# Kernel optimization log

Hardware: AMD Instinct MI355X
Metric: run time of the kernel (lower is better)

The kernel has to match this reference:

```python
import jax, jax.numpy as jnp
import numpy as np

B, S, H = 128, 1024, 256
NEG = 1e9

def setup_inputs() -> dict:
    key = jax.random.key(0)
    ks = jax.random.split(key, 11)
    sc = 0.05
    return {
        'ref': jax.random.normal(ks[0], (B, S, H), jnp.float32),
        'query': jax.random.normal(ks[1], (B, H), jnp.float32),
        'mask': jax.random.randint(ks[2], (B, S), 0, 2, jnp.int32),
        'wg': jax.random.normal(ks[3], (H, H), jnp.float32) * sc,
        'bg': jax.random.normal(ks[4], (H,), jnp.float32) * sc,
        'wqg': jax.random.normal(ks[5], (H, H), jnp.float32) * sc,
        'vg': jax.random.normal(ks[6], (H,), jnp.float32) * sc,
        'wp': jax.random.normal(ks[7], (H, H), jnp.float32) * sc,
        'bp': jax.random.normal(ks[8], (H,), jnp.float32) * sc,
        'wqp': jax.random.normal(ks[9], (H, H), jnp.float32) * sc,
        'vp': jax.random.normal(ks[10], (H,), jnp.float32) * sc,
    }

def reference(ref, query, mask, wg, bg, wqg, vg, wp, bp, wqp, vp):
    # Bahdanau additive pointer attention with glimpse, per PointerDecoder.pointer_net
    maskf = mask.astype(ref.dtype)
    # glimpse attention
    enc_g = jnp.einsum('bsd,hd->bsh', ref, wg) + bg            # conv1d kernel=1
    q_g = jnp.einsum('bd,hd->bh', query, wqg)                   # w_q_g (no bias)
    scores_g = jnp.einsum('bsh,h->bs', jnp.tanh(enc_g + q_g[:, None, :]), vg)
    att_g = jax.nn.softmax(scores_g - maskf * NEG, axis=-1)     # [B,S]
    glimpse = jnp.einsum('bs,bsd->bd', att_g, ref) + query      # [B,H]
    # pointer scores
    enc_p = jnp.einsum('bsd,hd->bsh', ref, wp) + bp
    q_p = jnp.einsum('bd,hd->bh', glimpse, wqp)
    scores_p = jnp.einsum('bsh,h->bs', jnp.tanh(enc_p + q_p[:, None, :]), vp)
    masked_scores = scores_p - maskf * NEG                      # [B,S]
    return masked_scores
```

## Files before the change

kernel.cpp:

```cpp
#include <hip/hip_runtime.h>

#define Bb 128
#define Ss 1024
#define Hh 256
#define NEGF 1e9f

typedef short bf16x8 __attribute__((ext_vector_type(8)));
typedef float f32x4 __attribute__((ext_vector_type(4)));

__device__ __forceinline__ short f2bf(float f) {
    union { float f; unsigned u; } c; c.f = f;
    return (short)((c.u + 0x8000u) >> 16);
}

__device__ __forceinline__ unsigned pack2bf(float lo, float hi) {
    union { float f; unsigned u; } a, b; a.f = lo; b.f = hi;
    unsigned al = (a.u + 0x8000u) >> 16;
    unsigned bh = (b.u + 0x8000u) & 0xFFFF0000u;
    return al | bh;
}

__device__ __forceinline__ float bfhi2f(unsigned u) {
    union { unsigned u; float f; } c; c.u = u & 0xFFFF0000u; return c.f;
}
__device__ __forceinline__ float bflo2f(unsigned u) {
    union { unsigned u; float f; } c; c.u = u << 16; return c.f;
}

__device__ __forceinline__ float fast_tanh(float x) {
    float cl = fminf(fmaxf(x, -10.f), 10.f);
    float e = __expf(2.f * cl);
    return (e - 1.f) * __builtin_amdgcn_rcpf(e + 1.f);
}

__device__ __forceinline__ void stage16(const short* g, short* l) {
    __builtin_amdgcn_global_load_lds((const __attribute__((address_space(1))) void*)g,
                                     (__attribute__((address_space(3))) void*)l, 16, 0, 0);
}

__global__ __launch_bounds__(256) void convert_ref(const float* __restrict__ ref,
                                                   uint4* __restrict__ refb) {
    size_t i = (size_t)blockIdx.x * 256 + threadIdx.x;
    const float4* p = (const float4*)ref + i * 2;
    float4 a = p[0], b = p[1];
    uint4 o;
    o.x = pack2bf(a.x, a.y);
    o.y = pack2bf(a.z, a.w);
    o.z = pack2bf(b.x, b.y);
    o.w = pack2bf(b.z, b.w);
    refb[i] = o;
}

__global__ __launch_bounds__(256) void convert_w(const float* __restrict__ wg,
                                                 const float* __restrict__ wp,
                                                 short* __restrict__ wgb,
                                                 short* __restrict__ wpb) {
    int i = blockIdx.x * 256 + threadIdx.x;
    wgb[i] = f2bf(wg[i]);
    wpb[i] = f2bf(wp[i]);
}

__global__ __launch_bounds__(256) void dot_qb(const float* __restrict__ q,
                                              const float* __restrict__ W,
                                              const float* __restrict__ bias,
                                              float* __restrict__ out) {
    int b = blockIdx.x, h = threadIdx.x;
    const float4* qr = (const float4*)(q + b * Hh);
    const float4* wr = (const float4*)(W + h * Hh);
    float acc = 0.f;
#pragma unroll 8
    for (int i = 0; i < Hh / 4; ++i) {
        float4 q4 = qr[i], w4 = wr[i];
        acc += q4.x * w4.x + q4.y * w4.y + q4.z * w4.z + q4.w * w4.w;
    }
    out[b * Hh + h] = acc + bias[h];
}

template <int MASKED>
__global__ __launch_bounds__(256) void scores_mfma(const short* __restrict__ refb,
                                                   const short* __restrict__ Wbf,
                                                   const float* __restrict__ qbias,
                                                   const float* __restrict__ vvec,
                                                   const int* __restrict__ mask,
                                                   float* __restrict__ out) {
    __shared__ short Wlds[2][8192];
    const int b = blockIdx.x;
    const int s0 = blockIdx.y * 128;
    const int t = threadIdx.x;
    const int wave = t >> 6;
    const int lane = t & 63;
    const int nl = lane & 15;
    const int quad = lane >> 4;
    const int rowbase = s0 + wave * 32;

    const int soff0 = (t & 15) * Hh + (t >> 6) * 32 + ((t >> 4) & 3) * 8;
    const int soff1 = soff0 + 128;
    const int dbase0 = wave * 512;
    const int dbase1 = 2048 + wave * 512;

    bf16x8 afrag[2][8];
#pragma unroll
    for (int rt = 0; rt < 2; ++rt) {
        const short* rp = refb + ((size_t)b * Ss + rowbase + rt * 16 + nl) * Hh;
#pragma unroll
        for (int kb = 0; kb < 8; ++kb)
            afrag[rt][kb] = *(const bf16x8*)(rp + kb * 32 + quad * 8);
    }

    stage16(Wbf + soff0, &Wlds[0][dbase0]);
    stage16(Wbf + soff1, &Wlds[0][dbase1]);
    stage16(Wbf + 16 * Hh + soff0, &Wlds[0][4096 + dbase0]);
    stage16(Wbf + 16 * Hh + soff1, &Wlds[0][4096 + dbase1]);
    __syncthreads();

    float sc[2][4] = {{0.f, 0.f, 0.f, 0.f}, {0.f, 0.f, 0.f, 0.f}};

    for (int nc2 = 0; nc2 < 8; ++nc2) {
        const int cur = nc2 & 1;
        if (nc2 < 7) {
            const short* g = Wbf + (size_t)(nc2 + 1) * 32 * Hh;
            stage16(g + soff0, &Wlds[1 - cur][dbase0]);
            stage16(g + soff1, &Wlds[1 - cur][dbase1]);
            stage16(g + 16 * Hh + soff0, &Wlds[1 - cur][4096 + dbase0]);
            stage16(g + 16 * Hh + soff1, &Wlds[1 - cur][4096 + dbase1]);
        }
#pragma unroll
        for (int h = 0; h < 2; ++h) {
            const int n = nc2 * 32 + h * 16 + nl;
            const float qb = qbias[b * Hh + n];
            const float vv = vvec[n];
            bf16x8 bfrag[8];
#pragma unroll
            for (int kb = 0; kb < 8; ++kb)
                bfrag[kb] = *(const bf16x8*)&Wlds[cur][h * 4096 + kb * 512 + lane * 8];
#pragma unroll
            for (int rt = 0; rt < 2; ++rt) {
                f32x4 c = {0.f, 0.f, 0.f, 0.f};
#pragma unroll
                for (int kb = 0; kb < 8; ++kb)
                    c = __builtin_amdgcn_mfma_f32_16x16x32_bf16(afrag[rt][kb], bfrag[kb], c, 0, 0, 0);
#pragma unroll
                for (int r = 0; r < 4; ++r)
                    sc[rt][r] += fast_tanh(c[r] + qb) * vv;
            }
        }
        __syncthreads();
    }

#pragma unroll
    for (int rt = 0; rt < 2; ++rt)
#pragma unroll
        for (int r = 0; r < 4; ++r) {
            float v = sc[rt][r];
            v += __shfl_xor(v, 1, 64);
            v += __shfl_xor(v, 2, 64);
            v += __shfl_xor(v, 4, 64);
            v += __shfl_xor(v, 8, 64);
            sc[rt][r] = v;
        }

    if (nl == 0) {
#pragma unroll
        for (int rt = 0; rt < 2; ++rt)
#pragma unroll
            for (int r = 0; r < 4; ++r) {
                int m = rowbase + rt * 16 + quad * 4 + r;
                float v = sc[rt][r];
                if (MASKED) v -= (float)mask[b * Ss + m] * NEGF;
                out[(size_t)b * Ss + m] = v;
            }
    }
}

__global__ __launch_bounds__(1024) void softmax_kernel(const float* __restrict__ scores,
                                                       const int* __restrict__ mask,
                                                       float* __restrict__ att) {
    int b = blockIdx.x, t = threadIdx.x;
    __shared__ float red[16];
    int idx = b * Ss + t;
    float x = scores[idx] - (float)mask[idx] * NEGF;

    float m = x;
#pragma unroll
    for (int o = 1; o < 64; o <<= 1) m = fmaxf(m, __shfl_xor(m, o, 64));
    if ((t & 63) == 0) red[t >> 6] = m;
    __syncthreads();
    float M = red[0];
#pragma unroll
    for (int j = 1; j < 16; ++j) M = fmaxf(M, red[j]);
    __syncthreads();

    float e = __expf(x - M);
    float s = e;
#pragma unroll
    for (int o = 1; o < 64; o <<= 1) s += __shfl_xor(s, o, 64);
    if ((t & 63) == 0) red[t >> 6] = s;
    __syncthreads();
    float S = 0.f;
#pragma unroll
    for (int j = 0; j < 16; ++j) S += red[j];

    att[idx] = e * __builtin_amdgcn_rcpf(S);
}

__global__ __launch_bounds__(256) void glimpse_part(const unsigned* __restrict__ refb,
                                                    const float* __restrict__ att,
                                                    float* __restrict__ gpart) {
    int b = blockIdx.x, q = blockIdx.y, t = threadIdx.x;
    const int c = t & 31;
    const int rg = t >> 5;
    __shared__ float part[8][Hh];
    const unsigned* base = refb + ((size_t)(b * Ss + q * 128)) * (Hh / 2);
    const float* ap = att + b * Ss + q * 128;

    float acc[8] = {0.f, 0.f, 0.f, 0.f, 0.f, 0.f, 0.f, 0.f};
#pragma unroll 4
    for (int it = 0; it < 16; ++it) {
        int row = it * 8 + rg;
        float a = ap[row];
        uint4 v = *(const uint4*)(base + (size_t)row * (Hh / 2) + c * 4);
        acc[0] += a * bflo2f(v.x); acc[1] += a * bfhi2f(v.x);
        acc[2] += a * bflo2f(v.y); acc[3] += a * bfhi2f(v.y);
        acc[4] += a * bflo2f(v.z); acc[5] += a * bfhi2f(v.z);
        acc[6] += a * bflo2f(v.w); acc[7] += a * bfhi2f(v.w);
    }
#pragma unroll
    for (int j = 0; j < 8; ++j) part[rg][c * 8 + j] = acc[j];
    __syncthreads();
    float s = 0.f;
#pragma unroll
    for (int g = 0; g < 8; ++g) s += part[g][t];
    gpart[(size_t)(b * 8 + q) * Hh + t] = s;
}

__global__ __launch_bounds__(256) void qbias_p_kernel(const float* __restrict__ gpart,
                                                      const float* __restrict__ query,
                                                      const float* __restrict__ wqp,
                                                      const float* __restrict__ bp,
                                                      float* __restrict__ out) {
    int b = blockIdx.x, t = threadIdx.x;
    __shared__ __align__(16) float gl[Hh];
    float g = query[b * Hh + t];
#pragma unroll
    for (int q = 0; q < 8; ++q) g += gpart[(b * 8 + q) * Hh + t];
    gl[t] = g;
    __syncthreads();
    const float4* wr = (const float4*)(wqp + t * Hh);
    const float4* gp = (const float4*)gl;
    float acc = 0.f;
#pragma unroll 8
    for (int i = 0; i < Hh / 4; ++i) {
        float4 w4 = wr[i];
        float4 g4 = gp[i];
        acc += w4.x * g4.x + w4.y * g4.y + w4.z * g4.z + w4.w * g4.w;
    }
    out[b * Hh + t] = acc + bp[t];
}

extern "C" void kernel_launch(void* const* d_in, const int* in_sizes, int n_in,
                              void* d_out, int out_size, void* d_ws, size_t ws_size,
                              hipStream_t stream) {
    const float* ref   = (const float*)d_in[0];
    const float* query = (const float*)d_in[1];
    const int*   mask  = (const int*)d_in[2];
    const float* wg    = (const float*)d_in[3];
    const float* bg    = (const float*)d_in[4];
    const float* wqg   = (const float*)d_in[5];
    const float* vg    = (const float*)d_in[6];
    const float* wp    = (const float*)d_in[7];
    const float* bp    = (const float*)d_in[8];
    const float* wqp   = (const float*)d_in[9];
    const float* vp    = (const float*)d_in[10];
    float* out = (float*)d_out;

    char* ws = (char*)d_ws;
    short* ref_bf   = (short*)(ws + 0);
    size_t off = (size_t)Bb * Ss * Hh * 2;
    short* wg_bf    = (short*)(ws + off);               off += 131072;
    short* wp_bf    = (short*)(ws + off);               off += 131072;
    float* qbias_g  = (float*)(ws + off);               off += 131072;
    float* qbias_p  = (float*)(ws + off);               off += 131072;
    float* scores_g = (float*)(ws + off);               off += 524288;
    float* att      = (float*)(ws + off);               off += 524288;
    float* gpart    = (float*)(ws + off);

    convert_ref<<<(Bb * Ss * Hh) / 2048, 256, 0, stream>>>(ref, (uint4*)ref_bf);
    convert_w<<<Hh * Hh / 256, 256, 0, stream>>>(wg, wp, wg_bf, wp_bf);
    dot_qb<<<Bb, Hh, 0, stream>>>(query, wqg, bg, qbias_g);
    scores_mfma<0><<<dim3(Bb, Ss / 128), 256, 0, stream>>>(ref_bf, wg_bf, qbias_g, vg, nullptr, scores_g);
    softmax_kernel<<<Bb, Ss, 0, stream>>>(scores_g, mask, att);
    glimpse_part<<<dim3(Bb, 8), 256, 0, stream>>>((const unsigned*)ref_bf, att, gpart);
    qbias_p_kernel<<<Bb, Hh, 0, stream>>>(gpart, query, wqp, bp, qbias_p);
    scores_mfma<1><<<dim3(Bb, Ss / 128), 256, 0, stream>>>(ref_bf, wp_bf, qbias_p, vp, mask, out);
}
```

Baseline: 313.4 us.

## Fuse ref bf16 conversion into first score kernel and split N across waves

Drops the separate convert_ref kernel: the first score kernel now reads fp32 ref, packs it to bf16 into LDS and also writes the bf16 copy for later kernels. Each block now covers 32 rows, with the four waves splitting the 256 hidden outputs and reading W fragments straight from global/L2 instead of double-buffered LDS staging. Partial scores are summed across waves in shared memory. This removes one full read/write pass over ref but raises W traffic per block and needs an extra cross-wave reduction.

```diff
diff --git a/kernel.cpp b/kernel.cpp
--- a/kernel.cpp
+++ b/kernel.cpp
@@ -15,9 +15,7 @@
 
 __device__ __forceinline__ unsigned pack2bf(float lo, float hi) {
     union { float f; unsigned u; } a, b; a.f = lo; b.f = hi;
-    unsigned al = (a.u + 0x8000u) >> 16;
-    unsigned bh = (b.u + 0x8000u) & 0xFFFF0000u;
-    return al | bh;
+    return ((a.u + 0x8000u) >> 16) | ((b.u + 0x8000u) & 0xFFFF0000u);
 }
 
 __device__ __forceinline__ float bfhi2f(unsigned u) {
@@ -31,24 +29,6 @@
     float cl = fminf(fmaxf(x, -10.f), 10.f);
     float e = __expf(2.f * cl);
     return (e - 1.f) * __builtin_amdgcn_rcpf(e + 1.f);
-}
-
-__device__ __forceinline__ void stage16(const short* g, short* l) {
-    __builtin_amdgcn_global_load_lds((const __attribute__((address_space(1))) void*)g,
-                                     (__attribute__((address_space(3))) void*)l, 16, 0, 0);
-}
-
-__global__ __launch_bounds__(256) void convert_ref(const float* __restrict__ ref,
-                                                   uint4* __restrict__ refb) {
-    size_t i = (size_t)blockIdx.x * 256 + threadIdx.x;
-    const float4* p = (const float4*)ref + i * 2;
-    float4 a = p[0], b = p[1];
-    uint4 o;
-    o.x = pack2bf(a.x, a.y);
-    o.y = pack2bf(a.z, a.w);
-    o.z = pack2bf(b.x, b.y);
-    o.w = pack2bf(b.z, b.w);
-    refb[i] = o;
 }
 
 __global__ __launch_bounds__(256) void convert_w(const float* __restrict__ wg,
@@ -76,75 +56,79 @@
     out[b * Hh + h] = acc + bias[h];
 }
 
-template <int MASKED>
-__global__ __launch_bounds__(256) void scores_mfma(const short* __restrict__ refb,
-                                                   const short* __restrict__ Wbf,
-                                                   const float* __restrict__ qbias,
-                                                   const float* __restrict__ vvec,
-                                                   const int* __restrict__ mask,
-                                                   float* __restrict__ out) {
-    __shared__ short Wlds[2][8192];
+template <int MASKED, int LOADF32>
+__global__ __launch_bounds__(256, 2) void scores_v5(const float* __restrict__ reff,
+                                                    const unsigned* __restrict__ refb_in,
+                                                    unsigned* __restrict__ refb_out,
+                                                    const short* __restrict__ Wbf,
+                                                    const float* __restrict__ qbias,
+                                                    const float* __restrict__ vvec,
+                                                    const int* __restrict__ mask,
+                                                    float* __restrict__ out) {
+    __shared__ short A[32 * 264];
+    __shared__ float part[4][32];
     const int b = blockIdx.x;
-    const int s0 = blockIdx.y * 128;
+    const int s0 = blockIdx.y * 32;
     const int t = threadIdx.x;
-    const int wave = t >> 6;
-    const int lane = t & 63;
-    const int nl = lane & 15;
-    const int quad = lane >> 4;
-    const int rowbase = s0 + wave * 32;
-
-    const int soff0 = (t & 15) * Hh + (t >> 6) * 32 + ((t >> 4) & 3) * 8;
-    const int soff1 = soff0 + 128;
-    const int dbase0 = wave * 512;
-    const int dbase1 = 2048 + wave * 512;
-
-    bf16x8 afrag[2][8];
-#pragma unroll
-    for (int rt = 0; rt < 2; ++rt) {
-        const short* rp = refb + ((size_t)b * Ss + rowbase + rt * 16 + nl) * Hh;
+    const int wave = t >> 6, lane = t & 63, nl = lane & 15, quad = lane >> 4;
+
+    if (LOADF32) {
+        const float4* src = (const float4*)(reff + ((size_t)b * Ss + s0) * Hh);
+        unsigned* dst = refb_out + ((size_t)b * Ss + s0) * (Hh / 2);
+#pragma unroll
+        for (int i = 0; i < 8; ++i) {
+            int f4 = i * 256 + t;
+            float4 v = src[f4];
+            unsigned lo = pack2bf(v.x, v.y), hi = pack2bf(v.z, v.w);
+            int row = f4 >> 6, col4 = f4 & 63;
+            *(uint2*)&A[row * 264 + col4 * 4] = make_uint2(lo, hi);
+            *(uint2*)&dst[(size_t)f4 * 2] = make_uint2(lo, hi);
+        }
+    } else {
+        const uint4* src = (const uint4*)(refb_in + ((size_t)b * Ss + s0) * (Hh / 2));
+#pragma unroll
+        for (int i = 0; i < 4; ++i) {
+            int u4 = i * 256 + t;
+            uint4 v = src[u4];
+            int row = u4 >> 5, c = u4 & 31;
+            *(uint4*)&A[row * 264 + c * 8] = v;
+        }
+    }
+    __syncthreads();
+
+    bf16x8 af[2][8];
+#pragma unroll
+    for (int rt = 0; rt < 2; ++rt)
 #pragma unroll
         for (int kb = 0; kb < 8; ++kb)
-            afrag[rt][kb] = *(const bf16x8*)(rp + kb * 32 + quad * 8);
-    }
-
-    stage16(Wbf + soff0, &Wlds[0][dbase0]);
-    stage16(Wbf + soff1, &Wlds[0][dbase1]);
-    stage16(Wbf + 16 * Hh + soff0, &Wlds[0][4096 + dbase0]);
-    stage16(Wbf + 16 * Hh + soff1, &Wlds[0][4096 + dbase1]);
-    __syncthreads();
+            af[rt][kb] = *(const bf16x8*)&A[(rt * 16 + nl) * 264 + kb * 32 + quad * 8];
+
+    float qb[4], vv[4];
+#pragma unroll
+    for (int j = 0; j < 4; ++j) {
+        int n = wave * 64 + j * 16 + nl;
+        qb[j] = qbias[b * Hh + n];
+        vv[j] = vvec[n];
+    }
 
     float sc[2][4] = {{0.f, 0.f, 0.f, 0.f}, {0.f, 0.f, 0.f, 0.f}};
-
-    for (int nc2 = 0; nc2 < 8; ++nc2) {
-        const int cur = nc2 & 1;
-        if (nc2 < 7) {
-            const short* g = Wbf + (size_t)(nc2 + 1) * 32 * Hh;
-            stage16(g + soff0, &Wlds[1 - cur][dbase0]);
-            stage16(g + soff1, &Wlds[1 - cur][dbase1]);
-            stage16(g + 16 * Hh + soff0, &Wlds[1 - cur][4096 + dbase0]);
-            stage16(g + 16 * Hh + soff1, &Wlds[1 - cur][4096 + dbase1]);
-        }
-#pragma unroll
-        for (int h = 0; h < 2; ++h) {
-            const int n = nc2 * 32 + h * 16 + nl;
-            const float qb = qbias[b * Hh + n];
-            const float vv = vvec[n];
-            bf16x8 bfrag[8];
+#pragma unroll
+    for (int j = 0; j < 4; ++j) {
+        const short* wr = Wbf + (wave * 64 + j * 16 + nl) * Hh;
+        bf16x8 bf[8];
+#pragma unroll
+        for (int kb = 0; kb < 8; ++kb)
+            bf[kb] = *(const bf16x8*)(wr + kb * 32 + quad * 8);
+#pragma unroll
+        for (int rt = 0; rt < 2; ++rt) {
+            f32x4 c = {0.f, 0.f, 0.f, 0.f};
 #pragma unroll
             for (int kb = 0; kb < 8; ++kb)
-                bfrag[kb] = *(const bf16x8*)&Wlds[cur][h * 4096 + kb * 512 + lane * 8];
-#pragma unroll
-            for (int rt = 0; rt < 2; ++rt) {
-                f32x4 c = {0.f, 0.f, 0.f, 0.f};
-#pragma unroll
-                for (int kb = 0; kb < 8; ++kb)
-                    c = __builtin_amdgcn_mfma_f32_16x16x32_bf16(afrag[rt][kb], bfrag[kb], c, 0, 0, 0);
-#pragma unroll
-                for (int r = 0; r < 4; ++r)
-                    sc[rt][r] += fast_tanh(c[r] + qb) * vv;
-            }
-        }
-        __syncthreads();
+                c = __builtin_amdgcn_mfma_f32_16x16x32_bf16(af[rt][kb], bf[kb], c, 0, 0, 0);
+#pragma unroll
+            for (int r = 0; r < 4; ++r)
+                sc[rt][r] += fast_tanh(c[r] + qb[j]) * vv[j];
+        }
     }
 
 #pragma unroll
@@ -163,12 +147,15 @@
 #pragma unroll
         for (int rt = 0; rt < 2; ++rt)
 #pragma unroll
-            for (int r = 0; r < 4; ++r) {
-                int m = rowbase + rt * 16 + quad * 4 + r;
-                float v = sc[rt][r];
-                if (MASKED) v -= (float)mask[b * Ss + m] * NEGF;
-                out[(size_t)b * Ss + m] = v;
-            }
+            for (int r = 0; r < 4; ++r)
+                part[wave][rt * 16 + quad * 4 + r] = sc[rt][r];
+    }
+    __syncthreads();
+
+    if (t < 32) {
+        float x = part[0][t] + part[1][t] + part[2][t] + part[3][t];
+        if (MASKED) x -= (float)mask[b * Ss + s0 + t] * NEGF;
+        out[(size_t)b * Ss + s0 + t] = x;
     }
 }
 
@@ -284,12 +271,13 @@
     float* att      = (float*)(ws + off);               off += 524288;
     float* gpart    = (float*)(ws + off);
 
-    convert_ref<<<(Bb * Ss * Hh) / 2048, 256, 0, stream>>>(ref, (uint4*)ref_bf);
     convert_w<<<Hh * Hh / 256, 256, 0, stream>>>(wg, wp, wg_bf, wp_bf);
     dot_qb<<<Bb, Hh, 0, stream>>>(query, wqg, bg, qbias_g);
-    scores_mfma<0><<<dim3(Bb, Ss / 128), 256, 0, stream>>>(ref_bf, wg_bf, qbias_g, vg, nullptr, scores_g);
+    scores_v5<0, 1><<<dim3(Bb, Ss / 32), 256, 0, stream>>>(
+        ref, nullptr, (unsigned*)ref_bf, wg_bf, qbias_g, vg, nullptr, scores_g);
     softmax_kernel<<<Bb, Ss, 0, stream>>>(scores_g, mask, att);
     glimpse_part<<<dim3(Bb, 8), 256, 0, stream>>>((const unsigned*)ref_bf, att, gpart);
     qbias_p_kernel<<<Bb, Hh, 0, stream>>>(gpart, query, wqp, bp, qbias_p);
-    scores_mfma<1><<<dim3(Bb, Ss / 128), 256, 0, stream>>>(ref_bf, wp_bf, qbias_p, vp, mask, out);
-}
+    scores_v5<1, 0><<<dim3(Bb, Ss / 32), 256, 0, stream>>>(
+        nullptr, (const unsigned*)ref_bf, nullptr, wp_bf, qbias_p, vp, mask, out);
+}
```

New measurement: 365.6 us. +16.6%, slower.

## Fuse ref bf16 conversion into first scores kernel and merge prep kernels

Applied to the files above, without the earlier changes.

Removes the standalone convert_ref pass. The first scores_mfma now loads fp32 ref directly, converts each fragment to bf16 in registers, and writes the bf16 copy back for the later glimpse and pointer kernels. This drops one full read of ref_bf that the old separate conversion pass required. Weight conversion and the glimpse query-bias dot product are also merged into a single prep kernel, cutting launch count. The cost is that the first scores kernel now reads twice as many bytes and does extra stores, which may lengthen its critical path.

```diff
diff --git a/kernel.cpp b/kernel.cpp
--- a/kernel.cpp
+++ b/kernel.cpp
@@ -13,18 +13,20 @@
     return (short)((c.u + 0x8000u) >> 16);
 }
 
-__device__ __forceinline__ unsigned pack2bf(float lo, float hi) {
-    union { float f; unsigned u; } a, b; a.f = lo; b.f = hi;
-    unsigned al = (a.u + 0x8000u) >> 16;
-    unsigned bh = (b.u + 0x8000u) & 0xFFFF0000u;
-    return al | bh;
-}
-
 __device__ __forceinline__ float bfhi2f(unsigned u) {
     union { unsigned u; float f; } c; c.u = u & 0xFFFF0000u; return c.f;
 }
 __device__ __forceinline__ float bflo2f(unsigned u) {
     union { unsigned u; float f; } c; c.u = u << 16; return c.f;
+}
+
+__device__ __forceinline__ bf16x8 ld_bf8_f32(const float* p) {
+    const float4* p4 = (const float4*)p;
+    float4 a = p4[0], b = p4[1];
+    bf16x8 r;
+    r[0] = f2bf(a.x); r[1] = f2bf(a.y); r[2] = f2bf(a.z); r[3] = f2bf(a.w);
+    r[4] = f2bf(b.x); r[5] = f2bf(b.y); r[6] = f2bf(b.z); r[7] = f2bf(b.w);
+    return r;
 }
 
 __device__ __forceinline__ float fast_tanh(float x) {
@@ -38,46 +40,37 @@
                                      (__attribute__((address_space(3))) void*)l, 16, 0, 0);
 }
 
-__global__ __launch_bounds__(256) void convert_ref(const float* __restrict__ ref,
-                                                   uint4* __restrict__ refb) {
-    size_t i = (size_t)blockIdx.x * 256 + threadIdx.x;
-    const float4* p = (const float4*)ref + i * 2;
-    float4 a = p[0], b = p[1];
-    uint4 o;
-    o.x = pack2bf(a.x, a.y);
-    o.y = pack2bf(a.z, a.w);
-    o.z = pack2bf(b.x, b.y);
-    o.w = pack2bf(b.z, b.w);
-    refb[i] = o;
-}
-
-__global__ __launch_bounds__(256) void convert_w(const float* __restrict__ wg,
-                                                 const float* __restrict__ wp,
-                                                 short* __restrict__ wgb,
-                                                 short* __restrict__ wpb) {
-    int i = blockIdx.x * 256 + threadIdx.x;
-    wgb[i] = f2bf(wg[i]);
-    wpb[i] = f2bf(wp[i]);
-}
-
-__global__ __launch_bounds__(256) void dot_qb(const float* __restrict__ q,
-                                              const float* __restrict__ W,
-                                              const float* __restrict__ bias,
-                                              float* __restrict__ out) {
-    int b = blockIdx.x, h = threadIdx.x;
-    const float4* qr = (const float4*)(q + b * Hh);
-    const float4* wr = (const float4*)(W + h * Hh);
-    float acc = 0.f;
+__global__ __launch_bounds__(256) void prep_kernel(const float* __restrict__ wg,
+                                                   const float* __restrict__ wp,
+                                                   const float* __restrict__ query,
+                                                   const float* __restrict__ wqg,
+                                                   const float* __restrict__ bg,
+                                                   short* __restrict__ wgb,
+                                                   short* __restrict__ wpb,
+                                                   float* __restrict__ qbias_g) {
+    int blk = blockIdx.x, t = threadIdx.x;
+    if (blk < 256) {
+        int i = blk * 256 + t;
+        wgb[i] = f2bf(wg[i]);
+        wpb[i] = f2bf(wp[i]);
+    } else {
+        int b = blk - 256;
+        const float4* qr = (const float4*)(query + b * Hh);
+        const float4* wr = (const float4*)(wqg + t * Hh);
+        float acc = 0.f;
 #pragma unroll 8
-    for (int i = 0; i < Hh / 4; ++i) {
-        float4 q4 = qr[i], w4 = wr[i];
-        acc += q4.x * w4.x + q4.y * w4.y + q4.z * w4.z + q4.w * w4.w;
-    }
-    out[b * Hh + h] = acc + bias[h];
-}
-
-template <int MASKED>
-__global__ __launch_bounds__(256) void scores_mfma(const short* __restrict__ refb,
+        for (int i = 0; i < Hh / 4; ++i) {
+            float4 q4 = qr[i], w4 = wr[i];
+            acc += q4.x * w4.x + q4.y * w4.y + q4.z * w4.z + q4.w * w4.w;
+        }
+        qbias_g[b * Hh + t] = acc + bg[t];
+    }
+}
+
+template <int MASKED, int LOADF32>
+__global__ __launch_bounds__(256) void scores_mfma(const float* __restrict__ reff,
+                                                   const short* __restrict__ refb_in,
+                                                   short* __restrict__ refb_out,
                                                    const short* __restrict__ Wbf,
                                                    const float* __restrict__ qbias,
                                                    const float* __restrict__ vvec,
@@ -101,10 +94,22 @@
     bf16x8 afrag[2][8];
 #pragma unroll
     for (int rt = 0; rt < 2; ++rt) {
-        const short* rp = refb + ((size_t)b * Ss + rowbase + rt * 16 + nl) * Hh;
-#pragma unroll
-        for (int kb = 0; kb < 8; ++kb)
-            afrag[rt][kb] = *(const bf16x8*)(rp + kb * 32 + quad * 8);
+        const size_t rowoff = ((size_t)b * Ss + rowbase + rt * 16 + nl) * Hh;
+        if (LOADF32) {
+            const float* rp = reff + rowoff;
+#pragma unroll
+            for (int kb = 0; kb < 8; ++kb)
+                afrag[rt][kb] = ld_bf8_f32(rp + kb * 32 + quad * 8);
+            short* dst = refb_out + rowoff;
+#pragma unroll
+            for (int kb = 0; kb < 8; ++kb)
+                *(bf16x8*)(dst + kb * 32 + quad * 8) = afrag[rt][kb];
+        } else {
+            const short* rp = refb_in + rowoff;
+#pragma unroll
+            for (int kb = 0; kb < 8; ++kb)
+                afrag[rt][kb] = *(const bf16x8*)(rp + kb * 32 + quad * 8);
+        }
     }
 
     stage16(Wbf + soff0, &Wlds[0][dbase0]);
@@ -284,12 +289,12 @@
     float* att      = (float*)(ws + off);               off += 524288;
     float* gpart    = (float*)(ws + off);
 
-    convert_ref<<<(Bb * Ss * Hh) / 2048, 256, 0, stream>>>(ref, (uint4*)ref_bf);
-    convert_w<<<Hh * Hh / 256, 256, 0, stream>>>(wg, wp, wg_bf, wp_bf);
-    dot_qb<<<Bb, Hh, 0, stream>>>(query, wqg, bg, qbias_g);
-    scores_mfma<0><<<dim3(Bb, Ss / 128), 256, 0, stream>>>(ref_bf, wg_bf, qbias_g, vg, nullptr, scores_g);
+    prep_kernel<<<384, 256, 0, stream>>>(wg, wp, query, wqg, bg, wg_bf, wp_bf, qbias_g);
+    scores_mfma<0, 1><<<dim3(Bb, Ss / 128), 256, 0, stream>>>(
+        ref, nullptr, ref_bf, wg_bf, qbias_g, vg, nullptr, scores_g);
     softmax_kernel<<<Bb, Ss, 0, stream>>>(scores_g, mask, att);
     glimpse_part<<<dim3(Bb, 8), 256, 0, stream>>>((const unsigned*)ref_bf, att, gpart);
     qbias_p_kernel<<<Bb, Hh, 0, stream>>>(gpart, query, wqp, bp, qbias_p);
-    scores_mfma<1><<<dim3(Bb, Ss / 128), 256, 0, stream>>>(ref_bf, wp_bf, qbias_p, vp, mask, out);
-}
+    scores_mfma<1, 0><<<dim3(Bb, Ss / 128), 256, 0, stream>>>(
+        nullptr, ref_bf, nullptr, wp_bf, qbias_p, vp, mask, out);
+}
```

Result: faster. 298.3 us (-4.8%).
